# Kernel optimization log

Hardware: AMD Instinct MI355X
Metric: run time of the kernel (lower is better)

The kernel has to match this reference:

```python
import jax, jax.numpy as jnp
import numpy as np

B, L, H, N, O = 64, 512, 768, 50, 768
ALPHA = 0.3  # leaky relu slope in GAT
NEG_INF = -9e15


def _position_encoding(n, d):
    # standard sinusoidal PE, shape [n, d]
    pos = jnp.arange(n, dtype=jnp.float32)[:, None]              # [n,1]
    div = jnp.exp(jnp.arange(0, d, 2, dtype=jnp.float32) * (-np.log(10000.0) / d))  # [d/2]
    ang = pos * div[None, :]                                     # [n, d/2]
    return jnp.stack([jnp.sin(ang), jnp.cos(ang)], axis=-1).reshape(n, d)


def _gat_layer(x, adj, W, b, a, ab):
    # Dense GAT layer. Original builds an [N,N,2F] concat tensor then applies
    # linear a; mathematically identical to splitting a into src/dst halves.
    Wh = x @ W + b                                               # [N,F]
    Fdim = Wh.shape[-1]
    a_src = Wh @ a[:Fdim]                                        # [N]
    a_dst = Wh @ a[Fdim:]                                        # [N]
    e = jax.nn.leaky_relu(a_src[:, None] + a_dst[None, :] + ab, negative_slope=ALPHA)
    att = jax.nn.softmax(jnp.where(adj > 0, e, NEG_INF), axis=1)  # rows sum to 1
    return att @ Wh                                              # [N,F]


def setup_inputs() -> dict:
    key = jax.random.key(0)
    ks = jax.random.split(key, 16)
    s = 1.0 / np.sqrt(H)
    utter_embedding = jax.random.normal(ks[0], (B, L, H), jnp.float32)
    cls_ids = jnp.sort(jax.random.randint(ks[1], (B, N), 0, L), axis=1).astype(jnp.int32)
    adj = jax.random.randint(ks[2], (B, N, N), 0, 2).astype(jnp.int32)
    adj = adj | jnp.eye(N, dtype=jnp.int32)  # ensure self loops so softmax rows are valid
    return {
        "utter_embedding": utter_embedding,
        "cls_ids": cls_ids,
        "adj": adj,
        # GAT head 0 (concat=True)
        "W1": jax.random.normal(ks[3], (H, H), jnp.float32) * s,
        "b1": jnp.zeros((H,), jnp.float32),
        "a1": jax.random.normal(ks[4], (2 * H,), jnp.float32) * s,
        "ab1": jnp.zeros((), jnp.float32),
        # GAT out layer (concat=False)
        "W2": jax.random.normal(ks[5], (H, H), jnp.float32) * s,
        "b2": jnp.zeros((H,), jnp.float32),
        "a2": jax.random.normal(ks[6], (2 * H,), jnp.float32) * s,
        "ab2": jnp.zeros((), jnp.float32),
        # Attention pooling over utterances
        "Wa": jax.random.normal(ks[7], (H, H), jnp.float32) * s,
        "ba": jnp.zeros((H,), jnp.float32),
        "v": jax.random.normal(ks[8], (H,), jnp.float32) * s,
        # Final linear
        "Wl": jax.random.normal(ks[9], (H, O), jnp.float32) * s,
        "bl": jnp.zeros((O,), jnp.float32),
    }


def reference(utter_embedding, cls_ids, adj, W1, b1, a1, ab1, W2, b2, a2, ab2,
              Wa, ba, v, Wl, bl):
    pe = _position_encoding(N, H)                                # [N,H]

    def per_dialogue(emb, ids, A):
        # gather [CLS] utterance embeddings: index_select
        x = jnp.take(emb, ids, axis=0)                           # [N,H]
        x = x + pe                                               # position encoder
        # GAT: 1 head concat -> elu, out layer -> elu, residual
        h = jax.nn.elu(_gat_layer(x, A, W1, b1, a1, ab1))
        h = jax.nn.elu(_gat_layer(h, A, W2, b2, a2, ab2)) + x    # residual per GAT.forward
        # attention pooling over N utterances
        scores = jax.nn.softmax(jnp.tanh(h @ Wa + ba) @ v, axis=0)  # [N]
        return scores @ h                                        # [H]

    dialogue = jax.vmap(per_dialogue)(utter_embedding, cls_ids, adj)  # [B,H]
    return dialogue @ Wl + bl                                    # [B,O]
```

## Files before the change

### kernel.cpp

```cpp
#include <hip/hip_runtime.h>
#include <hip/hip_bf16.h>
#include <math.h>

typedef __attribute__((ext_vector_type(8))) short bf16x8;
typedef __attribute__((ext_vector_type(4))) float f32x4;

constexpr int Bn = 64;
constexpr int Ln = 512;
constexpr int Hd = 768;
constexpr int Nn = 50;
constexpr int On = 768;

struct PrepArgs {
  const float* src[4];
  __hip_bfloat16* dst[4];
  float* aux;
  int auxn;
};

__global__ __launch_bounds__(256) void prep_kernel(PrepArgs args) {
  int job = blockIdx.y;
  if (job < 4) {
    __shared__ float tile[32][33];
    int t = blockIdx.x;
    int bx = (t % 24) * 32, by = (t / 24) * 32;
    const float* W = args.src[job];
    __hip_bfloat16* Wt = args.dst[job];
    int c = threadIdx.x & 31, r0 = threadIdx.x >> 5;
    for (int r = r0; r < 32; r += 8)
      tile[r][c] = W[(size_t)(bx + r) * Hd + by + c];
    __syncthreads();
    for (int r = r0; r < 32; r += 8)
      Wt[(size_t)(by + r) * Hd + bx + c] = __float2bfloat16(tile[c][r]);
  } else {
    int idx = blockIdx.x * 256 + threadIdx.x;
    if (idx < args.auxn) args.aux[idx] = 0.f;
  }
}

__global__ __launch_bounds__(256) void gather_pe_kernel(
    const float* __restrict__ emb, const int* __restrict__ ids,
    float* __restrict__ xf, __hip_bfloat16* __restrict__ xb) {
  int bn = blockIdx.x;
  int b = bn / Nn, n = bn % Nn;
  int id = ids[bn];
  const float* src = emb + ((size_t)b * Ln + id) * Hd;
  float* xo = xf + (size_t)bn * Hd;
  __hip_bfloat16* xbo = xb + (size_t)bn * Hd;
  const float kLog = 9.210340371976184f / (float)Hd;
  for (int h = threadIdx.x; h < Hd; h += 256) {
    int he = h & ~1;
    float freq = expf(-(float)he * kLog);
    float ang = (float)n * freq;
    float pe = (h & 1) ? cosf(ang) : sinf(ang);
    float v = src[h] + pe;
    xo[h] = v;
    xbo[h] = __float2bfloat16(v);
  }
}

template <int EPI>
__global__ __launch_bounds__(256) void gemm_kernel(
    const __hip_bfloat16* __restrict__ A, const __hip_bfloat16* __restrict__ Bt,
    const float* __restrict__ bias, float* __restrict__ C,
    const float* __restrict__ avec, float* __restrict__ o1,
    float* __restrict__ o2) {
  __shared__ __hip_bfloat16 As[64][40];
  __shared__ __hip_bfloat16 Bs[64][40];
  int tid = threadIdx.x;
  int wave = tid >> 6, lane = tid & 63;
  int lr = lane & 15, lq = lane >> 4;
  int row0 = blockIdx.x * 64, col0 = blockIdx.y * 64;
  int sr = tid >> 2, sk = (tid & 3) * 8;
  const __hip_bfloat16* Ap = A + (size_t)(row0 + sr) * Hd + sk;
  const __hip_bfloat16* Bp = Bt + (size_t)(col0 + sr) * Hd + sk;
  f32x4 acc[4] = {};
  for (int kt = 0; kt < Hd; kt += 32) {
    *(uint4*)&As[sr][sk] = *(const uint4*)(Ap + kt);
    *(uint4*)&Bs[sr][sk] = *(const uint4*)(Bp + kt);
    __syncthreads();
    bf16x8 af = *(const bf16x8*)&As[wave * 16 + lr][lq * 8];
#pragma unroll
    for (int ct = 0; ct < 4; ++ct) {
      bf16x8 bfrag = *(const bf16x8*)&Bs[ct * 16 + lr][lq * 8];
      acc[ct] = __builtin_amdgcn_mfma_f32_16x16x32_bf16(af, bfrag, acc[ct], 0, 0, 0);
    }
    __syncthreads();
  }
  int cr0 = row0 + wave * 16 + lq * 4;
  if (EPI == 0) {
    float ps[4] = {}, pd[4] = {};
#pragma unroll
    for (int ct = 0; ct < 4; ++ct) {
      int gc = col0 + ct * 16 + lr;
      float bv = bias[gc];
      float as_ = avec[gc], ad_ = avec[Hd + gc];
#pragma unroll
      for (int r = 0; r < 4; ++r) {
        float v = acc[ct][r] + bv;
        C[(size_t)(cr0 + r) * Hd + gc] = v;
        ps[r] += v * as_;
        pd[r] += v * ad_;
      }
    }
#pragma unroll
    for (int off = 8; off; off >>= 1)
#pragma unroll
      for (int r = 0; r < 4; ++r) {
        ps[r] += __shfl_xor(ps[r], off);
        pd[r] += __shfl_xor(pd[r], off);
      }
    if (lr == 0)
#pragma unroll
      for (int r = 0; r < 4; ++r) {
        atomicAdd(&o1[cr0 + r], ps[r]);
        atomicAdd(&o2[cr0 + r], pd[r]);
      }
  } else {
    float pr[4] = {};
#pragma unroll
    for (int ct = 0; ct < 4; ++ct) {
      int gc = col0 + ct * 16 + lr;
      float bv = bias[gc];
      float vv_ = avec[gc];
#pragma unroll
      for (int r = 0; r < 4; ++r) {
        float t = tanhf(acc[ct][r] + bv);
        pr[r] += t * vv_;
      }
    }
#pragma unroll
    for (int off = 8; off; off >>= 1)
#pragma unroll
      for (int r = 0; r < 4; ++r) pr[r] += __shfl_xor(pr[r], off);
    if (lr == 0)
#pragma unroll
      for (int r = 0; r < 4; ++r) atomicAdd(&o1[cr0 + r], pr[r]);
  }
}

template <int LAYER>
__global__ __launch_bounds__(256) void attf_kernel(
    const float* __restrict__ ssrc, const float* __restrict__ sdst,
    const int* __restrict__ adj, const float* __restrict__ ab,
    const float* __restrict__ Wh, const float* __restrict__ xres,
    float* __restrict__ hf, __hip_bfloat16* __restrict__ hb) {
  int b = blockIdx.y, h0 = blockIdx.x * 128;
  __shared__ float attL[Nn * Nn];
  float abv = ab[0];
  for (int idx = threadIdx.x; idx < Nn * Nn; idx += 256) {
    int i = idx / Nn, j = idx - i * Nn;
    float t = ssrc[b * Nn + i] + sdst[b * Nn + j] + abv;
    t = t > 0.f ? t : 0.3f * t;
    attL[idx] = (adj[(size_t)b * Nn * Nn + idx] > 0) ? t : -9.0e15f;
  }
  __syncthreads();
  if (threadIdx.x < Nn) {
    int i = threadIdx.x;
    float m = -3.0e38f;
    for (int j = 0; j < Nn; ++j) m = fmaxf(m, attL[i * Nn + j]);
    float s = 0.f;
    for (int j = 0; j < Nn; ++j) {
      float p = expf(attL[i * Nn + j] - m);
      attL[i * Nn + j] = p;
      s += p;
    }
    float inv = 1.f / s;
    for (int j = 0; j < Nn; ++j) attL[i * Nn + j] *= inv;
  }
  __syncthreads();
  int col = threadIdx.x & 127, half = threadIdx.x >> 7;
  int i0 = half * 25;
  float acc[25] = {};
  const float* Whb = Wh + ((size_t)b * Nn) * Hd + h0 + col;
  for (int j = 0; j < Nn; j += 2) {
    float w0 = Whb[(size_t)j * Hd];
    float w1 = Whb[(size_t)(j + 1) * Hd];
#pragma unroll
    for (int ii = 0; ii < 25; ++ii) {
      float2 a2 = *(const float2*)&attL[(i0 + ii) * Nn + j];
      acc[ii] += a2.x * w0 + a2.y * w1;
    }
  }
#pragma unroll
  for (int ii = 0; ii < 25; ++ii) {
    float v = acc[ii];
    v = v > 0.f ? v : expf(v) - 1.f;
    size_t off = ((size_t)b * Nn + i0 + ii) * Hd + h0 + col;
    if (LAYER == 2) {
      v += xres[off];
      hf[off] = v;
    }
    hb[off] = __float2bfloat16(v);
  }
}

__global__ __launch_bounds__(256) void poolfinal_kernel(
    const float* __restrict__ sraw, const float* __restrict__ h2,
    const __hip_bfloat16* __restrict__ Wlt, const float* __restrict__ bl,
    float* __restrict__ out) {
  int b = blockIdx.x;
  __shared__ float sc[Nn];
  __shared__ float ds[Hd];
  if (threadIdx.x < 64) {
    int j = threadIdx.x;
    float e = (j < Nn) ? sraw[b * Nn + j] : -3.0e38f;
    float m = e;
#pragma unroll
    for (int off = 32; off; off >>= 1) m = fmaxf(m, __shfl_xor(m, off));
    float p = (j < Nn) ? expf(e - m) : 0.f;
    float s = p;
#pragma unroll
    for (int off = 32; off; off >>= 1) s += __shfl_xor(s, off);
    if (j < Nn) sc[j] = p / s;
  }
  __syncthreads();
  for (int h = threadIdx.x; h < Hd; h += 256) {
    float a = 0.f;
#pragma unroll 10
    for (int j = 0; j < Nn; ++j) a += sc[j] * h2[((size_t)b * Nn + j) * Hd + h];
    ds[h] = a;
  }
  __syncthreads();
  for (int oo = 0; oo < 3; ++oo) {
    int o = oo * 256 + threadIdx.x;
    float acc = bl[o];
    const uint4* wr = (const uint4*)(Wlt + (size_t)o * Hd);
    for (int kk = 0; kk < Hd / 8; ++kk) {
      union { uint4 u; unsigned short s[8]; } w;
      w.u = wr[kk];
#pragma unroll
      for (int t = 0; t < 8; ++t)
        acc += ds[kk * 8 + t] * __uint_as_float((unsigned)w.s[t] << 16);
    }
    out[(size_t)b * On + o] = acc;
  }
}

extern "C" void kernel_launch(void* const* d_in, const int* in_sizes, int n_in,
                              void* d_out, int out_size, void* d_ws, size_t ws_size,
                              hipStream_t stream) {
  const float* emb = (const float*)d_in[0];
  const int* ids = (const int*)d_in[1];
  const int* adj = (const int*)d_in[2];
  const float* W1 = (const float*)d_in[3];
  const float* b1 = (const float*)d_in[4];
  const float* a1 = (const float*)d_in[5];
  const float* ab1 = (const float*)d_in[6];
  const float* W2 = (const float*)d_in[7];
  const float* b2 = (const float*)d_in[8];
  const float* a2 = (const float*)d_in[9];
  const float* ab2 = (const float*)d_in[10];
  const float* Wa = (const float*)d_in[11];
  const float* ba = (const float*)d_in[12];
  const float* vv = (const float*)d_in[13];
  const float* Wl = (const float*)d_in[14];
  const float* bl = (const float*)d_in[15];
  float* out = (float*)d_out;

  char* p = (char*)d_ws;
  auto alloc = [&](size_t bytes) {
    char* r = p;
    p += (bytes + 255) & ~(size_t)255;
    return r;
  };
  __hip_bfloat16* Wt1 = (__hip_bfloat16*)alloc((size_t)Hd * Hd * 2);
  __hip_bfloat16* Wt2 = (__hip_bfloat16*)alloc((size_t)Hd * Hd * 2);
  __hip_bfloat16* Wta = (__hip_bfloat16*)alloc((size_t)Hd * Hd * 2);
  __hip_bfloat16* Wlt = (__hip_bfloat16*)alloc((size_t)Hd * On * 2);
  float* aux = (float*)alloc(5 * Bn * Nn * 4);
  float* ssrc1 = aux;
  float* sdst1 = aux + Bn * Nn;
  float* ssrc2 = aux + 2 * Bn * Nn;
  float* sdst2 = aux + 3 * Bn * Nn;
  float* sraw = aux + 4 * Bn * Nn;
  float* xf = (float*)alloc((size_t)Bn * Nn * Hd * 4);
  __hip_bfloat16* xb = (__hip_bfloat16*)alloc((size_t)Bn * Nn * Hd * 2);
  float* Wh = (float*)alloc((size_t)Bn * Nn * Hd * 4);
  float* h2f = (float*)alloc((size_t)Bn * Nn * Hd * 4);
  __hip_bfloat16* hb = (__hip_bfloat16*)alloc((size_t)Bn * Nn * Hd * 2);

  PrepArgs pa;
  pa.src[0] = W1; pa.src[1] = W2; pa.src[2] = Wa; pa.src[3] = Wl;
  pa.dst[0] = Wt1; pa.dst[1] = Wt2; pa.dst[2] = Wta; pa.dst[3] = Wlt;
  pa.aux = aux; pa.auxn = 5 * Bn * Nn;
  prep_kernel<<<dim3(576, 5), 256, 0, stream>>>(pa);

  gather_pe_kernel<<<Bn * Nn, 256, 0, stream>>>(emb, ids, xf, xb);

  dim3 ggrid(Bn * Nn / 64, Hd / 64);
  dim3 agrid(Hd / 128, Bn);

  gemm_kernel<0><<<ggrid, 256, 0, stream>>>(xb, Wt1, b1, Wh, a1, ssrc1, sdst1);
  attf_kernel<1><<<agrid, 256, 0, stream>>>(ssrc1, sdst1, adj, ab1, Wh,
                                            nullptr, nullptr, hb);
  gemm_kernel<0><<<ggrid, 256, 0, stream>>>(hb, Wt2, b2, Wh, a2, ssrc2, sdst2);
  attf_kernel<2><<<agrid, 256, 0, stream>>>(ssrc2, sdst2, adj, ab2, Wh,
                                            xf, h2f, hb);
  gemm_kernel<1><<<ggrid, 256, 0, stream>>>(hb, Wta, ba, nullptr, vv, sraw,
                                            nullptr);
  poolfinal_kernel<<<Bn, 256, 0, stream>>>(sraw, h2f, Wlt, bl, out);
}
```

Before: 313.3 us.

## Fuse all stages into one persistent cooperative kernel with grid syncs

Replaces the six separate kernel launches with a single persistent cooperative kernel. Its blocks loop over the tiles of each stage (weight transpose, gather+PE, three GEMMs, two attention stages, pooling) and separate the stages with grid.sync. This removes launch overhead and inter-kernel gaps. In exchange the grid is capped by occupancy, at most 600 blocks with two per CU, so stages with many tiles get serialized, and each grid sync has its own cost. A fallback multi-kernel path is kept in case cooperative launch is unavailable.

Result: slower. 1.022 ms (+226.2%).

```diff
diff --git a/kernel.cpp b/kernel.cpp
--- a/kernel.cpp
+++ b/kernel.cpp
@@ -1,6 +1,9 @@
 #include <hip/hip_runtime.h>
+#include <hip/hip_cooperative_groups.h>
 #include <hip/hip_bf16.h>
 #include <math.h>
+
+namespace cg = cooperative_groups;
 
 typedef __attribute__((ext_vector_type(8))) short bf16x8;
 typedef __attribute__((ext_vector_type(4))) float f32x4;
@@ -11,37 +14,24 @@
 constexpr int Nn = 50;
 constexpr int On = 768;
 
-struct PrepArgs {
-  const float* src[4];
-  __hip_bfloat16* dst[4];
-  float* aux;
-  int auxn;
-};
-
-__global__ __launch_bounds__(256) void prep_kernel(PrepArgs args) {
-  int job = blockIdx.y;
-  if (job < 4) {
-    __shared__ float tile[32][33];
-    int t = blockIdx.x;
-    int bx = (t % 24) * 32, by = (t / 24) * 32;
-    const float* W = args.src[job];
-    __hip_bfloat16* Wt = args.dst[job];
-    int c = threadIdx.x & 31, r0 = threadIdx.x >> 5;
-    for (int r = r0; r < 32; r += 8)
-      tile[r][c] = W[(size_t)(bx + r) * Hd + by + c];
-    __syncthreads();
-    for (int r = r0; r < 32; r += 8)
-      Wt[(size_t)(by + r) * Hd + bx + c] = __float2bfloat16(tile[c][r]);
-  } else {
-    int idx = blockIdx.x * 256 + threadIdx.x;
-    if (idx < args.auxn) args.aux[idx] = 0.f;
-  }
-}
-
-__global__ __launch_bounds__(256) void gather_pe_kernel(
-    const float* __restrict__ emb, const int* __restrict__ ids,
-    float* __restrict__ xf, __hip_bfloat16* __restrict__ xb) {
-  int bn = blockIdx.x;
+
+__device__ __forceinline__ void transpose_tile(const float* W,
+                                               __hip_bfloat16* Wt, int t,
+                                               char* smem) {
+  float(*tile)[33] = (float(*)[33])smem;
+  int bx = (t % 24) * 32, by = (t / 24) * 32;
+  int c = threadIdx.x & 31, r0 = threadIdx.x >> 5;
+  for (int r = r0; r < 32; r += 8)
+    tile[r][c] = W[(size_t)(bx + r) * Hd + by + c];
+  __syncthreads();
+  for (int r = r0; r < 32; r += 8)
+    Wt[(size_t)(by + r) * Hd + bx + c] = __float2bfloat16(tile[c][r]);
+  __syncthreads();
+}
+
+__device__ __forceinline__ void gather_pe_row(const float* emb, const int* ids,
+                                              float* xf, __hip_bfloat16* xb,
+                                              int bn) {
   int b = bn / Nn, n = bn % Nn;
   int id = ids[bn];
   const float* src = emb + ((size_t)b * Ln + id) * Hd;
@@ -60,17 +50,15 @@
 }
 
 template <int EPI>
-__global__ __launch_bounds__(256) void gemm_kernel(
-    const __hip_bfloat16* __restrict__ A, const __hip_bfloat16* __restrict__ Bt,
-    const float* __restrict__ bias, float* __restrict__ C,
-    const float* __restrict__ avec, float* __restrict__ o1,
-    float* __restrict__ o2) {
-  __shared__ __hip_bfloat16 As[64][40];
-  __shared__ __hip_bfloat16 Bs[64][40];
+__device__ __forceinline__ void gemm_tile(
+    const __hip_bfloat16* A, const __hip_bfloat16* Bt, const float* bias,
+    float* C, const float* avec, float* o1, float* o2, int row0, int col0,
+    char* smem) {
+  __hip_bfloat16(*As)[40] = (__hip_bfloat16(*)[40])smem;
+  __hip_bfloat16(*Bs)[40] = (__hip_bfloat16(*)[40])(smem + 5120);
   int tid = threadIdx.x;
   int wave = tid >> 6, lane = tid & 63;
   int lr = lane & 15, lq = lane >> 4;
-  int row0 = blockIdx.x * 64, col0 = blockIdx.y * 64;
   int sr = tid >> 2, sk = (tid & 3) * 8;
   const __hip_bfloat16* Ap = A + (size_t)(row0 + sr) * Hd + sk;
   const __hip_bfloat16* Bp = Bt + (size_t)(col0 + sr) * Hd + sk;
@@ -140,13 +128,11 @@
 }
 
 template <int LAYER>
-__global__ __launch_bounds__(256) void attf_kernel(
-    const float* __restrict__ ssrc, const float* __restrict__ sdst,
-    const int* __restrict__ adj, const float* __restrict__ ab,
-    const float* __restrict__ Wh, const float* __restrict__ xres,
-    float* __restrict__ hf, __hip_bfloat16* __restrict__ hb) {
-  int b = blockIdx.y, h0 = blockIdx.x * 128;
-  __shared__ float attL[Nn * Nn];
+__device__ __forceinline__ void attf_tile(
+    const float* ssrc, const float* sdst, const int* adj, const float* ab,
+    const float* Wh, const float* xres, float* hf, __hip_bfloat16* hb, int b,
+    int h0, char* smem) {
+  float* attL = (float*)smem;
   float abv = ab[0];
   for (int idx = threadIdx.x; idx < Nn * Nn; idx += 256) {
     int i = idx / Nn, j = idx - i * Nn;
@@ -193,15 +179,14 @@
     }
     hb[off] = __float2bfloat16(v);
   }
-}
-
-__global__ __launch_bounds__(256) void poolfinal_kernel(
-    const float* __restrict__ sraw, const float* __restrict__ h2,
-    const __hip_bfloat16* __restrict__ Wlt, const float* __restrict__ bl,
-    float* __restrict__ out) {
-  int b = blockIdx.x;
-  __shared__ float sc[Nn];
-  __shared__ float ds[Hd];
+  __syncthreads();
+}
+
+__device__ __forceinline__ void poolfinal_tile(
+    const float* sraw, const float* h2, const __hip_bfloat16* Wlt,
+    const float* bl, float* out, int b, char* smem) {
+  float* sc = (float*)smem;
+  float* ds = (float*)(smem + 256);
   if (threadIdx.x < 64) {
     int j = threadIdx.x;
     float e = (j < Nn) ? sraw[b * Nn + j] : -3.0e38f;
@@ -235,69 +220,226 @@
     }
     out[(size_t)b * On + o] = acc;
   }
+  __syncthreads();
+}
+
+struct MegaArgs {
+  const float* emb; const int* ids; const int* adj;
+  const float* W1; const float* b1; const float* a1; const float* ab1;
+  const float* W2; const float* b2; const float* a2; const float* ab2;
+  const float* Wa; const float* ba; const float* vv;
+  const float* Wl; const float* bl;
+  float* out;
+  __hip_bfloat16 *Wt1, *Wt2, *Wta, *Wlt;
+  float* aux;
+  float *xf, *Wh, *h2f;
+  __hip_bfloat16 *xb, *hb;
+};
+
+__global__ __launch_bounds__(256, 2) void mega_kernel(MegaArgs a) {
+  cg::grid_group grid = cg::this_grid();
+  __shared__ alignas(16) char smem[10496];
+  const int G = gridDim.x;
+
+  {
+    const float* src[4] = {a.W1, a.W2, a.Wa, a.Wl};
+    __hip_bfloat16* dst[4] = {a.Wt1, a.Wt2, a.Wta, a.Wlt};
+    for (int t = blockIdx.x; t < 4 * 576; t += G)
+      transpose_tile(src[t / 576], dst[t / 576], t % 576, smem);
+    for (int bn = blockIdx.x; bn < Bn * Nn; bn += G)
+      gather_pe_row(a.emb, a.ids, a.xf, a.xb, bn);
+    for (int i = blockIdx.x * 256 + threadIdx.x; i < 5 * Bn * Nn; i += G * 256)
+      a.aux[i] = 0.f;
+  }
+  float* ssrc1 = a.aux;
+  float* sdst1 = a.aux + Bn * Nn;
+  float* ssrc2 = a.aux + 2 * Bn * Nn;
+  float* sdst2 = a.aux + 3 * Bn * Nn;
+  float* sraw = a.aux + 4 * Bn * Nn;
+  __threadfence();
+  grid.sync();
+
+  for (int t = blockIdx.x; t < 600; t += G)
+    gemm_tile<0>(a.xb, a.Wt1, a.b1, a.Wh, a.a1, ssrc1, sdst1, (t % 50) * 64,
+                 (t / 50) * 64, smem);
+  __threadfence();
+  grid.sync();
+
+  for (int t = blockIdx.x; t < 6 * Bn; t += G)
+    attf_tile<1>(ssrc1, sdst1, a.adj, a.ab1, a.Wh, nullptr, nullptr, a.hb,
+                 t / 6, (t % 6) * 128, smem);
+  __threadfence();
+  grid.sync();
+
+  for (int t = blockIdx.x; t < 600; t += G)
+    gemm_tile<0>(a.hb, a.Wt2, a.b2, a.Wh, a.a2, ssrc2, sdst2, (t % 50) * 64,
+                 (t / 50) * 64, smem);
+  __threadfence();
+  grid.sync();
+
+  for (int t = blockIdx.x; t < 6 * Bn; t += G)
+    attf_tile<2>(ssrc2, sdst2, a.adj, a.ab2, a.Wh, a.xf, a.h2f, a.hb, t / 6,
+                 (t % 6) * 128, smem);
+  __threadfence();
+  grid.sync();
+
+  for (int t = blockIdx.x; t < 600; t += G)
+    gemm_tile<1>(a.hb, a.Wta, a.ba, nullptr, a.vv, sraw, nullptr, (t % 50) * 64,
+                 (t / 50) * 64, smem);
+  __threadfence();
+  grid.sync();
+
+  for (int b = blockIdx.x; b < Bn; b += G)
+    poolfinal_tile(sraw, a.h2f, a.Wlt, a.bl, a.out, b, smem);
+}
+
+
+struct PrepArgs {
+  const float* src[4];
+  __hip_bfloat16* dst[4];
+  float* aux;
+  int auxn;
+};
+
+__global__ __launch_bounds__(256) void prep_kernel(PrepArgs args) {
+  __shared__ alignas(16) char smem[4352];
+  int job = blockIdx.y;
+  if (job < 4) {
+    transpose_tile(args.src[job], args.dst[job], blockIdx.x, smem);
+  } else {
+    int idx = blockIdx.x * 256 + threadIdx.x;
+    if (idx < args.auxn) args.aux[idx] = 0.f;
+  }
+}
+
+__global__ __launch_bounds__(256) void gather_pe_kernel(
+    const float* __restrict__ emb, const int* __restrict__ ids,
+    float* __restrict__ xf, __hip_bfloat16* __restrict__ xb) {
+  gather_pe_row(emb, ids, xf, xb, blockIdx.x);
+}
+
+template <int EPI>
+__global__ __launch_bounds__(256) void gemm_kernel(
+    const __hip_bfloat16* __restrict__ A, const __hip_bfloat16* __restrict__ Bt,
+    const float* __restrict__ bias, float* __restrict__ C,
+    const float* __restrict__ avec, float* __restrict__ o1,
+    float* __restrict__ o2) {
+  __shared__ alignas(16) char smem[10240];
+  gemm_tile<EPI>(A, Bt, bias, C, avec, o1, o2, blockIdx.x * 64,
+                 blockIdx.y * 64, smem);
+}
+
+template <int LAYER>
+__global__ __launch_bounds__(256) void attf_kernel(
+    const float* __restrict__ ssrc, const float* __restrict__ sdst,
+    const int* __restrict__ adj, const float* __restrict__ ab,
+    const float* __restrict__ Wh, const float* __restrict__ xres,
+    float* __restrict__ hf, __hip_bfloat16* __restrict__ hb) {
+  __shared__ alignas(16) char smem[10016];
+  attf_tile<LAYER>(ssrc, sdst, adj, ab, Wh, xres, hf, hb, blockIdx.x / 6,
+                   (blockIdx.x % 6) * 128, smem);
+}
+
+__global__ __launch_bounds__(256) void poolfinal_kernel(
+    const float* __restrict__ sraw, const float* __restrict__ h2,
+    const __hip_bfloat16* __restrict__ Wlt, const float* __restrict__ bl,
+    float* __restrict__ out) {
+  __shared__ alignas(16) char smem[3584];
+  poolfinal_tile(sraw, h2, Wlt, bl, out, blockIdx.x, smem);
 }
 
 extern "C" void kernel_launch(void* const* d_in, const int* in_sizes, int n_in,
                               void* d_out, int out_size, void* d_ws, size_t ws_size,
                               hipStream_t stream) {
-  const float* emb = (const float*)d_in[0];
-  const int* ids = (const int*)d_in[1];
-  const int* adj = (const int*)d_in[2];
-  const float* W1 = (const float*)d_in[3];
-  const float* b1 = (const float*)d_in[4];
-  const float* a1 = (const float*)d_in[5];
-  const float* ab1 = (const float*)d_in[6];
-  const float* W2 = (const float*)d_in[7];
-  const float* b2 = (const float*)d_in[8];
-  const float* a2 = (const float*)d_in[9];
-  const float* ab2 = (const float*)d_in[10];
-  const float* Wa = (const float*)d_in[11];
-  const float* ba = (const float*)d_in[12];
-  const float* vv = (const float*)d_in[13];
-  const float* Wl = (const float*)d_in[14];
-  const float* bl = (const float*)d_in[15];
-  float* out = (float*)d_out;
-
   char* p = (char*)d_ws;
   auto alloc = [&](size_t bytes) {
     char* r = p;
     p += (bytes + 255) & ~(size_t)255;
     return r;
   };
-  __hip_bfloat16* Wt1 = (__hip_bfloat16*)alloc((size_t)Hd * Hd * 2);
-  __hip_bfloat16* Wt2 = (__hip_bfloat16*)alloc((size_t)Hd * Hd * 2);
-  __hip_bfloat16* Wta = (__hip_bfloat16*)alloc((size_t)Hd * Hd * 2);
-  __hip_bfloat16* Wlt = (__hip_bfloat16*)alloc((size_t)Hd * On * 2);
-  float* aux = (float*)alloc(5 * Bn * Nn * 4);
-  float* ssrc1 = aux;
-  float* sdst1 = aux + Bn * Nn;
-  float* ssrc2 = aux + 2 * Bn * Nn;
-  float* sdst2 = aux + 3 * Bn * Nn;
-  float* sraw = aux + 4 * Bn * Nn;
-  float* xf = (float*)alloc((size_t)Bn * Nn * Hd * 4);
-  __hip_bfloat16* xb = (__hip_bfloat16*)alloc((size_t)Bn * Nn * Hd * 2);
-  float* Wh = (float*)alloc((size_t)Bn * Nn * Hd * 4);
-  float* h2f = (float*)alloc((size_t)Bn * Nn * Hd * 4);
-  __hip_bfloat16* hb = (__hip_bfloat16*)alloc((size_t)Bn * Nn * Hd * 2);
-
-  PrepArgs pa;
-  pa.src[0] = W1; pa.src[1] = W2; pa.src[2] = Wa; pa.src[3] = Wl;
-  pa.dst[0] = Wt1; pa.dst[1] = Wt2; pa.dst[2] = Wta; pa.dst[3] = Wlt;
-  pa.aux = aux; pa.auxn = 5 * Bn * Nn;
-  prep_kernel<<<dim3(576, 5), 256, 0, stream>>>(pa);
-
-  gather_pe_kernel<<<Bn * Nn, 256, 0, stream>>>(emb, ids, xf, xb);
-
-  dim3 ggrid(Bn * Nn / 64, Hd / 64);
-  dim3 agrid(Hd / 128, Bn);
-
-  gemm_kernel<0><<<ggrid, 256, 0, stream>>>(xb, Wt1, b1, Wh, a1, ssrc1, sdst1);
-  attf_kernel<1><<<agrid, 256, 0, stream>>>(ssrc1, sdst1, adj, ab1, Wh,
-                                            nullptr, nullptr, hb);
-  gemm_kernel<0><<<ggrid, 256, 0, stream>>>(hb, Wt2, b2, Wh, a2, ssrc2, sdst2);
-  attf_kernel<2><<<agrid, 256, 0, stream>>>(ssrc2, sdst2, adj, ab2, Wh,
-                                            xf, h2f, hb);
-  gemm_kernel<1><<<ggrid, 256, 0, stream>>>(hb, Wta, ba, nullptr, vv, sraw,
-                                            nullptr);
-  poolfinal_kernel<<<Bn, 256, 0, stream>>>(sraw, h2f, Wlt, bl, out);
-}
+  MegaArgs a;
+  a.emb = (const float*)d_in[0];
+  a.ids = (const int*)d_in[1];
+  a.adj = (const int*)d_in[2];
+  a.W1 = (const float*)d_in[3];  a.b1 = (const float*)d_in[4];
+  a.a1 = (const float*)d_in[5];  a.ab1 = (const float*)d_in[6];
+  a.W2 = (const float*)d_in[7];  a.b2 = (const float*)d_in[8];
+  a.a2 = (const float*)d_in[9];  a.ab2 = (const float*)d_in[10];
+  a.Wa = (const float*)d_in[11]; a.ba = (const float*)d_in[12];
+  a.vv = (const float*)d_in[13];
+  a.Wl = (const float*)d_in[14]; a.bl = (const float*)d_in[15];
+  a.out = (float*)d_out;
+
+  a.Wt1 = (__hip_bfloat16*)alloc((size_t)Hd * Hd * 2);
+  a.Wt2 = (__hip_bfloat16*)alloc((size_t)Hd * Hd * 2);
+  a.Wta = (__hip_bfloat16*)alloc((size_t)Hd * Hd * 2);
+  a.Wlt = (__hip_bfloat16*)alloc((size_t)Hd * On * 2);
+  a.aux = (float*)alloc(5 * Bn * Nn * 4);
+  a.xf = (float*)alloc((size_t)Bn * Nn * Hd * 4);
+  a.xb = (__hip_bfloat16*)alloc((size_t)Bn * Nn * Hd * 2);
+  a.Wh = (float*)alloc((size_t)Bn * Nn * Hd * 4);
+  a.h2f = (float*)alloc((size_t)Bn * Nn * Hd * 4);
+  a.hb = (__hip_bfloat16*)alloc((size_t)Bn * Nn * Hd * 2);
+
+  bool coop_ok = false;
+  int grid = 0;
+  {
+    int dev = 0;
+    (void)hipGetDevice(&dev);
+    int attr = 0;
+    if (hipDeviceGetAttribute(&attr, hipDeviceAttributeCooperativeLaunch,
+                              dev) == hipSuccess && attr) {
+      int numCU = 0, maxB = 0;
+      if (hipDeviceGetAttribute(&numCU,
+                                hipDeviceAttributeMultiprocessorCount,
+                                dev) == hipSuccess &&
+          hipOccupancyMaxActiveBlocksPerMultiprocessor(&maxB, mega_kernel, 256,
+                                                       0) == hipSuccess) {
+        grid = maxB * numCU;
+        if (grid > 600) grid = 600;
+        if (grid >= 64) coop_ok = true;
+      }
+    }
+  }
+
+  if (coop_ok) {
+    void* params[] = {(void*)&a};
+    hipError_t err = hipLaunchCooperativeKernel(
+        mega_kernel, dim3(grid), dim3(256), params, 0, stream);
+    if (err != hipSuccess) {
+      (void)hipGetLastError();
+      coop_ok = false;
+    }
+  }
+
+  if (!coop_ok) {
+    float* ssrc1 = a.aux;
+    float* sdst1 = a.aux + Bn * Nn;
+    float* ssrc2 = a.aux + 2 * Bn * Nn;
+    float* sdst2 = a.aux + 3 * Bn * Nn;
+    float* sraw = a.aux + 4 * Bn * Nn;
+
+    PrepArgs pa;
+    pa.src[0] = a.W1; pa.src[1] = a.W2; pa.src[2] = a.Wa; pa.src[3] = a.Wl;
+    pa.dst[0] = a.Wt1; pa.dst[1] = a.Wt2; pa.dst[2] = a.Wta; pa.dst[3] = a.Wlt;
+    pa.aux = a.aux; pa.auxn = 5 * Bn * Nn;
+    prep_kernel<<<dim3(576, 5), 256, 0, stream>>>(pa);
+
+    gather_pe_kernel<<<Bn * Nn, 256, 0, stream>>>(a.emb, a.ids, a.xf, a.xb);
+
+    dim3 ggrid(Bn * Nn / 64, Hd / 64);
+    dim3 agrid(6 * Bn);
+
+    gemm_kernel<0><<<ggrid, 256, 0, stream>>>(a.xb, a.Wt1, a.b1, a.Wh, a.a1,
+                                              ssrc1, sdst1);
+    attf_kernel<1><<<agrid, 256, 0, stream>>>(ssrc1, sdst1, a.adj, a.ab1, a.Wh,
+                                              nullptr, nullptr, a.hb);
+    gemm_kernel<0><<<ggrid, 256, 0, stream>>>(a.hb, a.Wt2, a.b2, a.Wh, a.a2,
+                                              ssrc2, sdst2);
+    attf_kernel<2><<<agrid, 256, 0, stream>>>(ssrc2, sdst2, a.adj, a.ab2, a.Wh,
+                                              a.xf, a.h2f, a.hb);
+    gemm_kernel<1><<<ggrid, 256, 0, stream>>>(a.hb, a.Wta, a.ba, nullptr, a.vv,
+                                              sraw, nullptr);
+    poolfinal_kernel<<<Bn, 256, 0, stream>>>(sraw, a.h2f, a.Wlt, a.bl, a.out);
+  }
+}
```
